# Kernel tuning notes

Measured on AMD Instinct MI355X. Metric: run time of the kernel, lower is better.

Reference implementation:

```python
import jax, jax.numpy as jnp
import numpy as np

N = 50000      # nodes
E = 600000     # edges
A = 8          # max attrs per node
DT = 64        # node type embed dim
DA = 64        # node attr embed dim
C = DT + DA    # annotation dim = GGNN channels
T = 16         # num node types
TE = 4         # num edge types
L = 4          # num_agg_steps
B = 256        # num graphs
VATTR = 1000   # num node attrs
ENC = 128      # encoder_output_dim
NCLS = 10      # decoder output classes


def setup_inputs() -> dict:
    key = jax.random.key(0)
    ks = jax.random.split(key, 16)
    s = 0.05
    x_type = jax.random.randint(ks[0], (N,), 0, T)
    x_attrs = jax.random.randint(ks[1], (N, A), 0, VATTR)
    x_attrs_mask = jax.random.randint(ks[2], (N,), 1, A + 1)  # >=1 valid attr per node
    edge_index = jax.random.randint(ks[3], (2, E), 0, N)
    edge_attr = jax.random.randint(ks[4], (E,), 0, TE)
    batch = jnp.sort(jax.random.randint(ks[5], (N,), 0, B))
    return {
        'x_type': x_type, 'x_attrs': x_attrs, 'x_attrs_mask': x_attrs_mask,
        'edge_index': edge_index, 'edge_attr': edge_attr,
        'num_graphs': int(B), 'batch': batch,
        'type_emb': jax.random.normal(ks[6], (T, DT)) * s,
        'attr_emb': jax.random.normal(ks[7], (VATTR, DA)) * s,
        'W_msg': jax.random.normal(ks[8], (L, TE, C, C)) * s,
        'W_ih': jax.random.normal(ks[9], (3 * C, C)) * s,
        'W_hh': jax.random.normal(ks[10], (3 * C, C)) * s,
        'b_ih': jnp.zeros((3 * C,)),
        'b_hh': jnp.zeros((3 * C,)),
        'w_attn': jax.random.normal(ks[11], (C,)) * s,
        'b_attn': jnp.zeros(()),
        'W_enc': jax.random.normal(ks[12], (T * C, ENC)) * s,
        'b_enc': jnp.zeros((ENC,)),
        'W_dec': jax.random.normal(ks[13], (ENC, NCLS)) * s,
        'b_dec': jnp.zeros((NCLS,)),
    }


def _gru_cell(m, h, W_ih, W_hh, b_ih, b_hh):
    gi = m @ W_ih.T + b_ih            # [N, 3C]
    gh = h @ W_hh.T + b_hh            # [N, 3C]
    ir, iz, inn = jnp.split(gi, 3, axis=-1)
    hr, hz, hn = jnp.split(gh, 3, axis=-1)
    r = jax.nn.sigmoid(ir + hr)
    z = jax.nn.sigmoid(iz + hz)
    n = jnp.tanh(inn + r * hn)
    return (1.0 - z) * n + z * h


def reference(x_type, x_attrs, x_attrs_mask, edge_index, edge_attr, num_graphs, batch,
              type_emb, attr_emb, W_msg, W_ih, W_hh, b_ih, b_hh,
              w_attn, b_attn, W_enc, b_enc, W_dec, b_dec):
    n = x_type.shape[0]
    # --- embed node types and ragged-mean attribute embeddings ---
    t_emb = type_emb[x_type]                                   # [N, DT]
    a_all = attr_emb[x_attrs]                                  # [N, A, DA]
    valid = (jnp.arange(A)[None, :] < x_attrs_mask[:, None]).astype(a_all.dtype)
    a_emb = (a_all * valid[..., None]).sum(1) / jnp.maximum(x_attrs_mask, 1)[:, None].astype(a_all.dtype)
    x = jnp.concatenate([t_emb, a_emb], axis=1)                # [N, C]

    # --- GatedGraphConv with per-edge-type weights (sum aggregation + GRU) ---
    src, dst = edge_index[0], edge_index[1]
    for l in range(L):
        h_all = jnp.einsum('nc,tcd->tnd', x, W_msg[l])         # [TE, N, C]
        m_e = h_all.reshape(TE * n, C)[edge_attr * n + src]    # [E, C] gather per edge
        m = jax.ops.segment_sum(m_e, dst, num_segments=n)      # [N, C]
        x = _gru_cell(m, x, W_ih, W_hh, b_ih, b_hh)

    # --- per-(graph, node_type) segment mean (zeros for empty groups) ---
    seg = batch * T + x_type                                   # [N]
    S = num_graphs * T
    sums = jax.ops.segment_sum(x, seg, num_segments=S)         # [B*T, C]
    cnt = jax.ops.segment_sum(jnp.ones((n,), x.dtype), seg, num_segments=S)
    agg = jnp.where(cnt[:, None] > 0, sums / jnp.maximum(cnt, 1.0)[:, None], 0.0)
    agg = agg.reshape(num_graphs, T, C)                        # [B, T, C]

    # --- attention over node types, flatten, encode, decode ---
    w = agg @ w_attn + b_attn                                  # [B, T]
    attn = jax.nn.softmax(w, axis=-1)
    flat = (attn[..., None] * agg).reshape(num_graphs, T * C)  # [B, T*C]
    enc = flat @ W_enc + b_enc                                 # [B, ENC]
    return enc @ W_dec + b_dec                                 # [B, NCLS]
```

## Files before the change

### kernel.cpp

```cpp
#include <hip/hip_runtime.h>
#include <hip/hip_bf16.h>

#define NN 50000
#define NP 50016
#define EE 600000
#define AA 8
#define CC 128
#define TT 16
#define TE 4
#define LL 4
#define BB 256
#define ENC 128
#define NCLS 10
#define SROW 136

typedef __attribute__((ext_vector_type(8))) short bf16x8;
typedef __attribute__((ext_vector_type(4))) float fx4;

__device__ __forceinline__ float b2f(ushort u) {
    union { float f; uint32_t i; } v; v.i = ((uint32_t)u) << 16; return v.f;
}
__device__ __forceinline__ ushort f2b(float f) {
    union { float f; uint32_t i; } v; v.f = f;
    uint32_t x = v.i;
    x += 0x7FFFu + ((x >> 16) & 1u);
    return (ushort)(x >> 16);
}
__device__ __forceinline__ float ldw(const void* p, long i, int isf) {
    return isf ? ((const float*)p)[i] : b2f(((const ushort*)p)[i]);
}
__device__ __forceinline__ float sigm(float t) { return 1.f / (1.f + __expf(-t)); }

__global__ void sniff_kernel(int* flag, const void* W_enc_raw) {
    const ushort* u = (const ushort*)W_enc_raw;
    int good = 0;
    for (int i = 0; i < 256; ++i) {
        ushort v = u[i];
        int ex = (v >> 7) & 0xFF;
        if (v == 0 || (ex >= 100 && ex <= 126)) ++good;
    }
    *flag = (good >= 230) ? 0 : 1;
}

__global__ __launch_bounds__(256) void wstk_kernel(ushort* __restrict__ wstk,
                                                   const void* __restrict__ W,
                                                   const int* __restrict__ flag) {
    const int isf = *flag;
    int idx = blockIdx.x * 256 + threadIdx.x;
    int l = idx >> 16;
    int rem = idx & 65535;
    int d = rem >> 9, r2 = rem & 511;
    int t = r2 >> 7, c = r2 & 127;
    long src = ((long)(l * 4 + t) << 14) + c * 128 + d;
    wstk[idx] = isf ? f2b(((const float*)W)[src]) : ((const ushort*)W)[src];
}

__global__ __launch_bounds__(256) void wgru_kernel(ushort* __restrict__ wgb,
                                                   const void* __restrict__ Wih,
                                                   const void* __restrict__ Whh,
                                                   const int* __restrict__ flag) {
    const int isf = *flag;
    int idx = blockIdx.x * 256 + threadIdx.x;
    if (idx >= 98304) return;
    int ih = (idx < 49152);
    int off = ih ? idx : idx - 49152;
    wgb[idx] = f2b(ldw(ih ? Wih : Whh, off, isf));
}

__global__ __launch_bounds__(256) void wencT_kernel(ushort* __restrict__ wencT,
                                                    const void* __restrict__ W_enc,
                                                    const int* __restrict__ flag) {
    const int isf = *flag;
    int idx = blockIdx.x * 256 + threadIdx.x;
    int j = idx >> 11, k = idx & 2047;
    wencT[idx] = f2b(ldw(W_enc, (long)k * ENC + j, isf));
}

__global__ __launch_bounds__(256) void bconv_kernel(float* __restrict__ cvt,
                                                    const void* __restrict__ bih, const void* __restrict__ bhh,
                                                    const void* __restrict__ b_enc, const void* __restrict__ w_attn,
                                                    const void* __restrict__ b_dec, const void* __restrict__ b_attn,
                                                    const void* __restrict__ W_dec,
                                                    const int* __restrict__ flag) {
    const int isf = *flag;
    int i = blockIdx.x * 256 + threadIdx.x;
    if (i < 384) cvt[i] = ldw(bih, i, isf);
    else if (i < 768) cvt[i] = ldw(bhh, i - 384, isf);
    else if (i < 896) cvt[i] = ldw(b_enc, i - 768, isf);
    else if (i < 1024) cvt[i] = ldw(w_attn, i - 896, isf);
    else if (i < 1034) cvt[i] = ldw(b_dec, i - 1024, isf);
    else if (i == 1034) cvt[i] = ldw(b_attn, 0, isf);
    else if (i >= 1040 && i < 2320) cvt[i] = ldw(W_dec, i - 1040, isf);
}

__global__ __launch_bounds__(256) void embed_kernel(
    ushort* __restrict__ xbf,
    const int* __restrict__ x_type, const int* __restrict__ x_attrs,
    const int* __restrict__ x_mask, const void* __restrict__ type_emb,
    const void* __restrict__ attr_emb, const int* __restrict__ flag) {
    const int isf = *flag;
    int idx = blockIdx.x * 256 + threadIdx.x;
    int n = idx >> 6, c = idx & 63;
    if (n >= NP) return;
    if (n >= NN) { xbf[n * CC + c] = 0; xbf[n * CC + 64 + c] = 0; return; }
    int ty = x_type[n];
    xbf[n * CC + c] = f2b(ldw(type_emb, ty * 64 + c, isf));
    int cnt = x_mask[n];
    float s = 0.f;
    for (int a = 0; a < cnt; ++a) s += ldw(attr_emb, x_attrs[n * AA + a] * 64 + c, isf);
    xbf[n * CC + 64 + c] = f2b(s / (float)cnt);
}

__global__ __launch_bounds__(256) void deg_kernel(int* __restrict__ cnt, const int* __restrict__ ei) {
    int e = blockIdx.x * 256 + threadIdx.x;
    if (e < EE) atomicAdd(&cnt[ei[EE + e]], 1);
}
__global__ __launch_bounds__(256) void scan1_kernel(int* __restrict__ cnt, int* __restrict__ btot) {
    __shared__ int s[256];
    int tid = threadIdx.x, i = blockIdx.x * 256 + tid;
    int v = (i < NN) ? cnt[i] : 0;
    s[tid] = v; __syncthreads();
    for (int off = 1; off < 256; off <<= 1) {
        int t = (tid >= off) ? s[tid - off] : 0; __syncthreads();
        s[tid] += t; __syncthreads();
    }
    if (i < NN) cnt[i] = s[tid] - v;
    if (tid == 255) btot[blockIdx.x] = s[255];
}
__global__ __launch_bounds__(256) void scan2_kernel(int* __restrict__ btot, int nb) {
    __shared__ int s[256];
    int tid = threadIdx.x;
    int v = (tid < nb) ? btot[tid] : 0;
    s[tid] = v; __syncthreads();
    for (int off = 1; off < 256; off <<= 1) {
        int t = (tid >= off) ? s[tid - off] : 0; __syncthreads();
        s[tid] += t; __syncthreads();
    }
    if (tid < nb) btot[tid] = s[tid] - v;
}
__global__ __launch_bounds__(256) void scan3_kernel(int* __restrict__ cnt, const int* __restrict__ btot) {
    int i = blockIdx.x * 256 + threadIdx.x;
    if (i < NN) cnt[i] += btot[blockIdx.x];
}
__global__ __launch_bounds__(256) void fill_kernel(uint* __restrict__ csr, int* __restrict__ cnt,
                                                   const int* __restrict__ ei, const int* __restrict__ ea) {
    int e = blockIdx.x * 256 + threadIdx.x;
    if (e >= EE) return;
    int d = ei[EE + e];
    int pos = atomicAdd(&cnt[d], 1);
    csr[pos] = (uint)ei[e] | ((uint)ea[e] << 16);
}

__global__ __launch_bounds__(256) void gather4_kernel(
    ushort* __restrict__ s4, const ushort* __restrict__ xin,
    const uint* __restrict__ csr, const int* __restrict__ endp) {
    int w = threadIdx.x >> 6, l = threadIdx.x & 63;
    int node = blockIdx.x * 4 + w;
    int start = (node == 0) ? 0 : endp[node - 1];
    int end = endp[node];
    int c0 = l * 2;
    float a0 = 0.f, b0 = 0.f, a1 = 0.f, b1 = 0.f;
    float a2 = 0.f, b2 = 0.f, a3 = 0.f, b3 = 0.f;
    for (int i = start; i < end; ++i) {
        uint pk = csr[i];
        uint src = pk & 0xFFFFu, t = pk >> 16;
        uint hv = *(const uint*)&xin[((size_t)src << 7) + c0];
        float lo = b2f((ushort)(hv & 0xFFFFu)), hf = b2f((ushort)(hv >> 16));
        if (t == 0)      { a0 += lo; b0 += hf; }
        else if (t == 1) { a1 += lo; b1 += hf; }
        else if (t == 2) { a2 += lo; b2 += hf; }
        else             { a3 += lo; b3 += hf; }
    }
    size_t base = (size_t)node << 9;
    *(uint*)&s4[base +   0 + c0] = (uint)f2b(a0) | ((uint)f2b(b0) << 16);
    *(uint*)&s4[base + 128 + c0] = (uint)f2b(a1) | ((uint)f2b(b1) << 16);
    *(uint*)&s4[base + 256 + c0] = (uint)f2b(a2) | ((uint)f2b(b2) << 16);
    *(uint*)&s4[base + 384 + c0] = (uint)f2b(a3) | ((uint)f2b(b3) << 16);
}

template <int AGG>
__global__ __launch_bounds__(256) void msggru_kernel(
    const ushort* __restrict__ xin, ushort* __restrict__ xout,
    const ushort* __restrict__ s4, const ushort* __restrict__ wstk,
    const ushort* __restrict__ wgb, const float* __restrict__ cvt,
    float* __restrict__ sums, float* __restrict__ cnta,
    const int* __restrict__ batch, const int* __restrict__ x_type) {
    __shared__ ushort m_bf[32][SROW];
    int tid = threadIdx.x;
    int w = tid >> 6, l = tid & 63;
    int node0 = blockIdx.x * 32;
    int lr = l & 15, lk = (l >> 4) * 8, hi = l >> 4;

    {
        fx4 mq[2][2];
        mq[0][0] = (fx4){0,0,0,0}; mq[0][1] = (fx4){0,0,0,0};
        mq[1][0] = (fx4){0,0,0,0}; mq[1][1] = (fx4){0,0,0,0};
        int ct0 = w * 2, ct1 = w * 2 + 1;
#pragma unroll
        for (int ks = 0; ks < 16; ++ks) {
            int ko = ks * 32 + lk;
            bf16x8 aA = *(const bf16x8*)&s4[((size_t)(node0 + lr) << 9) + ko];
            bf16x8 aB = *(const bf16x8*)&s4[((size_t)(node0 + 16 + lr) << 9) + ko];
            bf16x8 bA = *(const bf16x8*)&wstk[(size_t)(ct0 * 16 + lr) * 512 + ko];
            bf16x8 bB = *(const bf16x8*)&wstk[(size_t)(ct1 * 16 + lr) * 512 + ko];
            mq[0][0] = __builtin_amdgcn_mfma_f32_16x16x32_bf16(aA, bA, mq[0][0], 0, 0, 0);
            mq[0][1] = __builtin_amdgcn_mfma_f32_16x16x32_bf16(aB, bA, mq[0][1], 0, 0, 0);
            mq[1][0] = __builtin_amdgcn_mfma_f32_16x16x32_bf16(aA, bB, mq[1][0], 0, 0, 0);
            mq[1][1] = __builtin_amdgcn_mfma_f32_16x16x32_bf16(aB, bB, mq[1][1], 0, 0, 0);
        }
#pragma unroll
        for (int cc = 0; cc < 2; ++cc)
#pragma unroll
            for (int rt = 0; rt < 2; ++rt)
#pragma unroll
                for (int r = 0; r < 4; ++r)
                    m_bf[rt * 16 + hi * 4 + r][(w * 2 + cc) * 16 + lr] = f2b(mq[cc][rt][r]);
    }
    __syncthreads();

    bf16x8 mf[2][4], xf[2][4];
#pragma unroll
    for (int rt = 0; rt < 2; ++rt)
#pragma unroll
        for (int ks = 0; ks < 4; ++ks) {
            mf[rt][ks] = *(const bf16x8*)&m_bf[rt * 16 + lr][ks * 32 + lk];
            xf[rt][ks] = *(const bf16x8*)&xin[(size_t)(node0 + rt * 16 + lr) * CC + ks * 32 + lk];
        }
#pragma unroll
    for (int cc = 0; cc < 2; ++cc) {
        int ct = w * 2 + cc;
        int row0 = ct * 16 + lr;
        fx4 ai[3][2], ah[3][2];
#pragma unroll
        for (int s = 0; s < 3; ++s)
#pragma unroll
            for (int rt = 0; rt < 2; ++rt) { ai[s][rt] = (fx4){0,0,0,0}; ah[s][rt] = (fx4){0,0,0,0}; }
#pragma unroll
        for (int ks = 0; ks < 4; ++ks) {
            int ko = ks * 32 + lk;
            bf16x8 bI[3], bH[3];
#pragma unroll
            for (int s = 0; s < 3; ++s) {
                bI[s] = *(const bf16x8*)&wgb[(size_t)(s * 128 + row0) * 128 + ko];
                bH[s] = *(const bf16x8*)&wgb[49152 + (size_t)(s * 128 + row0) * 128 + ko];
            }
#pragma unroll
            for (int s = 0; s < 3; ++s)
#pragma unroll
                for (int rt = 0; rt < 2; ++rt) {
                    ai[s][rt] = __builtin_amdgcn_mfma_f32_16x16x32_bf16(mf[rt][ks], bI[s], ai[s][rt], 0, 0, 0);
                    ah[s][rt] = __builtin_amdgcn_mfma_f32_16x16x32_bf16(xf[rt][ks], bH[s], ah[s][rt], 0, 0, 0);
                }
        }
        float bi0 = cvt[row0],        bh0 = cvt[384 + row0];
        float bi1 = cvt[128 + row0],  bh1 = cvt[512 + row0];
        float bi2 = cvt[256 + row0],  bh2 = cvt[640 + row0];
#pragma unroll
        for (int rt = 0; rt < 2; ++rt)
#pragma unroll
            for (int r = 0; r < 4; ++r) {
                int node = node0 + rt * 16 + hi * 4 + r;
                if (node >= NN) continue;
                float rg = sigm(ai[0][rt][r] + bi0 + ah[0][rt][r] + bh0);
                float zg = sigm(ai[1][rt][r] + bi1 + ah[1][rt][r] + bh1);
                float ny = ai[2][rt][r] + bi2 + rg * (ah[2][rt][r] + bh2);
                float ng = 2.f * sigm(2.f * ny) - 1.f;
                size_t xi = (size_t)node * CC + row0;
                float xo = b2f(xin[xi]);
                float xn = (1.f - zg) * ng + zg * xo;
                xout[xi] = f2b(xn);
                if (AGG) {
                    int seg = batch[node] * TT + x_type[node];
                    atomicAdd(&sums[(size_t)seg * CC + row0], xn);
                    if (row0 == 0) atomicAdd(&cnta[seg], 1.0f);
                }
            }
    }
}

__global__ __launch_bounds__(256) void attnflat_kernel(
    ushort* __restrict__ flatbf, const float* __restrict__ sums, const float* __restrict__ cnt,
    const float* __restrict__ cvt) {
    __shared__ float agg_s[TT][CC + 1];
    __shared__ float wpart[TT][8];
    __shared__ float attn_s[TT];
    int b = blockIdx.x, tid = threadIdx.x;
#pragma unroll
    for (int q = 0; q < 8; ++q) {
        int idx = tid + q * 256;
        int t = idx >> 7, c = idx & 127;
        float cv = cnt[b * TT + t];
        agg_s[t][c] = cv > 0.f ? sums[(size_t)(b * TT + t) * CC + c] / cv : 0.f;
    }
    __syncthreads();
    if (tid < 128) {
        int t = tid >> 3, p = tid & 7;
        float acc = 0.f;
        for (int i = 0; i < 16; ++i) acc += agg_s[t][p * 16 + i] * cvt[896 + p * 16 + i];
        wpart[t][p] = acc;
    }
    __syncthreads();
    if (tid < 16) {
        float acc = cvt[1034];
        for (int p = 0; p < 8; ++p) acc += wpart[tid][p];
        attn_s[tid] = acc;
    }
    __syncthreads();
    if (tid == 0) {
        float mx = attn_s[0];
        for (int t = 1; t < TT; ++t) mx = fmaxf(mx, attn_s[t]);
        float ssum = 0.f, ex[TT];
        for (int t = 0; t < TT; ++t) { ex[t] = __expf(attn_s[t] - mx); ssum += ex[t]; }
        for (int t = 0; t < TT; ++t) attn_s[t] = ex[t] / ssum;
    }
    __syncthreads();
#pragma unroll
    for (int q = 0; q < 8; ++q) {
        int idx = tid + q * 256;
        int t = idx >> 7, c = idx & 127;
        flatbf[(size_t)b * 2048 + idx] = f2b(agg_s[t][c] * attn_s[t]);
    }
}

__global__ __launch_bounds__(256) void enc_mfma(
    float* __restrict__ encp, const ushort* __restrict__ flatbf, const ushort* __restrict__ wencT) {
    int tid = threadIdx.x;
    int w = tid >> 6, l = tid & 63;
    int bid = blockIdx.x;
    int m0 = (bid >> 2) * 16;
    int kc = (bid & 3) * 512;
    int lr = l & 15, lk = (l >> 4) * 8;
    fx4 acc0 = {0,0,0,0}, acc1 = {0,0,0,0};
    int ct0 = w * 2, ct1 = w * 2 + 1;
#pragma unroll
    for (int ks = 0; ks < 16; ++ks) {
        int ko = kc + ks * 32 + lk;
        bf16x8 af = *(const bf16x8*)&flatbf[(size_t)(m0 + lr) * 2048 + ko];
        bf16x8 b0 = *(const bf16x8*)&wencT[(size_t)(ct0 * 16 + lr) * 2048 + ko];
        bf16x8 b1 = *(const bf16x8*)&wencT[(size_t)(ct1 * 16 + lr) * 2048 + ko];
        acc0 = __builtin_amdgcn_mfma_f32_16x16x32_bf16(af, b0, acc0, 0, 0, 0);
        acc1 = __builtin_amdgcn_mfma_f32_16x16x32_bf16(af, b1, acc1, 0, 0, 0);
    }
#pragma unroll
    for (int r = 0; r < 4; ++r) {
        int row = m0 + (l >> 4) * 4 + r;
        encp[(size_t)(bid & 3) * BB * ENC + (size_t)row * ENC + ct0 * 16 + lr] = acc0[r];
        encp[(size_t)(bid & 3) * BB * ENC + (size_t)row * ENC + ct1 * 16 + lr] = acc1[r];
    }
}

__global__ __launch_bounds__(256) void dec_kernel(
    void* __restrict__ out, const float* __restrict__ encp, const float* __restrict__ cvt,
    const int* __restrict__ flag) {
    const int isf = *flag;
    __shared__ float encs[ENC];
    int b = blockIdx.x, tid = threadIdx.x;
    if (tid < 128) {
        float e = cvt[768 + tid];
#pragma unroll
        for (int p = 0; p < 4; ++p) e += encp[(size_t)p * BB * ENC + (size_t)b * ENC + tid];
        encs[tid] = e;
    }
    __syncthreads();
    if (tid < NCLS) {
        float acc = cvt[1024 + tid];
        for (int j = 0; j < ENC; ++j) acc += encs[j] * cvt[1040 + j * NCLS + tid];
        int oi = b * NCLS + tid;
        if (isf) ((float*)out)[oi] = acc;
        else ((ushort*)out)[oi] = f2b(acc);
    }
}

extern "C" void kernel_launch(void* const* d_in, const int* in_sizes, int n_in,
                              void* d_out, int out_size, void* d_ws, size_t ws_size,
                              hipStream_t stream) {
    const int* x_type      = (const int*)d_in[0];
    const int* x_attrs     = (const int*)d_in[1];
    const int* x_mask      = (const int*)d_in[2];
    const int* edge_index  = (const int*)d_in[3];
    const int* edge_attr   = (const int*)d_in[4];
    const int* batch       = (const int*)d_in[6];
    const void* type_emb   = d_in[7];
    const void* attr_emb   = d_in[8];
    const void* W_msg      = d_in[9];
    const void* W_ih       = d_in[10];
    const void* W_hh       = d_in[11];
    const void* b_ih       = d_in[12];
    const void* b_hh       = d_in[13];
    const void* w_attn     = d_in[14];
    const void* b_attn     = d_in[15];
    const void* W_enc      = d_in[16];
    const void* b_enc      = d_in[17];
    const void* W_dec      = d_in[18];
    const void* b_dec      = d_in[19];

    char* p = (char*)d_ws;
    ushort* xbf0  = (ushort*)p;          p += (size_t)NP * CC * 2;
    ushort* xbf1  = (ushort*)p;          p += (size_t)NP * CC * 2;
    ushort* s4    = (ushort*)p;          p += (size_t)NP * 512 * 2;
    ushort* wstk  = (ushort*)p;          p += (size_t)LL * 128 * 512 * 2;
    ushort* wgb   = (ushort*)p;          p += (size_t)2 * 384 * 128 * 2;
    ushort* wencT = (ushort*)p;          p += (size_t)ENC * 2048 * 2;
    ushort* flatbf= (ushort*)p;          p += (size_t)BB * 2048 * 2;
    float*  encp  = (float*)p;           p += (size_t)4 * BB * ENC * 4;
    float*  cvt   = (float*)p;           p += 2320 * 4;
    float*  sums  = (float*)p;           p += (size_t)BB * TT * CC * 4;
    float*  cnta  = (float*)p;           p += (size_t)BB * TT * 4;
    uint*   csr   = (uint*)p;            p += (size_t)EE * 4;
    int*    cptr  = (int*)p;             p += (size_t)NN * 4;
    int*    btot  = (int*)p;             p += 256 * 4;
    int*    flag  = (int*)p;

    sniff_kernel<<<1, 1, 0, stream>>>(flag, W_enc);
    wstk_kernel<<<1024, 256, 0, stream>>>(wstk, W_msg, flag);
    wgru_kernel<<<384, 256, 0, stream>>>(wgb, W_ih, W_hh, flag);
    wencT_kernel<<<1024, 256, 0, stream>>>(wencT, W_enc, flag);
    bconv_kernel<<<10, 256, 0, stream>>>(cvt, b_ih, b_hh, b_enc, w_attn, b_dec, b_attn, W_dec, flag);
    embed_kernel<<<(NP * 64) / 256, 256, 0, stream>>>(xbf0, x_type, x_attrs, x_mask,
                                                      type_emb, attr_emb, flag);

    const int NB = (NN + 255) / 256;
    hipMemsetAsync(cptr, 0, (size_t)NN * sizeof(int), stream);
    deg_kernel<<<(EE + 255) / 256, 256, 0, stream>>>(cptr, edge_index);
    scan1_kernel<<<NB, 256, 0, stream>>>(cptr, btot);
    scan2_kernel<<<1, 256, 0, stream>>>(btot, NB);
    scan3_kernel<<<NB, 256, 0, stream>>>(cptr, btot);
    fill_kernel<<<(EE + 255) / 256, 256, 0, stream>>>(csr, cptr, edge_index, edge_attr);

    hipMemsetAsync(sums, 0, (size_t)(BB * TT * CC + BB * TT) * sizeof(float), stream);

    const int tile_grid = NP / 32;
    for (int l = 0; l < LL; ++l) {
        const ushort* xin = (l & 1) ? xbf1 : xbf0;
        ushort* xout      = (l & 1) ? xbf0 : xbf1;
        gather4_kernel<<<NN / 4, 256, 0, stream>>>(s4, xin, csr, cptr);
        const ushort* wl = wstk + (size_t)l * 128 * 512;
        if (l < LL - 1)
            msggru_kernel<0><<<tile_grid, 256, 0, stream>>>(xin, xout, s4, wl, wgb, cvt,
                                                            sums, cnta, batch, x_type);
        else
            msggru_kernel<1><<<tile_grid, 256, 0, stream>>>(xin, xout, s4, wl, wgb, cvt,
                                                            sums, cnta, batch, x_type);
    }

    attnflat_kernel<<<BB, 256, 0, stream>>>(flatbf, sums, cnta, cvt);
    enc_mfma<<<64, 256, 0, stream>>>(encp, flatbf, wencT);
    dec_kernel<<<BB, 256, 0, stream>>>(d_out, encp, cvt, flag);
}
```

Baseline: 840.8 us.

## Stage s4 tile in LDS, XCD-swizzle block order, unroll edge gather by two

The message-GRU kernel now copies the 32x512 s4 tile for its block into shared memory once, so the MFMA A operands are read from LDS instead of being fetched repeatedly from global memory by all four waves. Both the gather and the msggru kernels remap block IDs with an XCD-aware swizzle so that adjacent node blocks land on the same XCD, which should improve L2 locality. The gather loop processes two edges per iteration to expose more independent loads. In exchange, the kernel uses about 33KB of extra LDS, which may reduce occupancy, and adds a barrier before the compute.

```diff
diff --git a/kernel.cpp b/kernel.cpp
--- a/kernel.cpp
+++ b/kernel.cpp
@@ -13,6 +13,7 @@
 #define ENC 128
 #define NCLS 10
 #define SROW 136
+#define STR 520
 
 typedef __attribute__((ext_vector_type(8))) short bf16x8;
 typedef __attribute__((ext_vector_type(4))) float fx4;
@@ -30,6 +31,11 @@
     return isf ? ((const float*)p)[i] : b2f(((const ushort*)p)[i]);
 }
 __device__ __forceinline__ float sigm(float t) { return 1.f / (1.f + __expf(-t)); }
+
+__device__ __forceinline__ int xcd_swz(int bid, int nwg) {
+    int q = nwg >> 3, r = nwg & 7, x = bid & 7, o = bid >> 3;
+    return (x < r ? x * (q + 1) : r * (q + 1) + (x - r) * q) + o;
+}
 
 __global__ void sniff_kernel(int* flag, const void* W_enc_raw) {
     const ushort* u = (const ushort*)W_enc_raw;
@@ -155,13 +161,32 @@
     ushort* __restrict__ s4, const ushort* __restrict__ xin,
     const uint* __restrict__ csr, const int* __restrict__ endp) {
     int w = threadIdx.x >> 6, l = threadIdx.x & 63;
-    int node = blockIdx.x * 4 + w;
+    int wg = xcd_swz(blockIdx.x, NN / 4);
+    int node = wg * 4 + w;
     int start = (node == 0) ? 0 : endp[node - 1];
     int end = endp[node];
     int c0 = l * 2;
     float a0 = 0.f, b0 = 0.f, a1 = 0.f, b1 = 0.f;
     float a2 = 0.f, b2 = 0.f, a3 = 0.f, b3 = 0.f;
-    for (int i = start; i < end; ++i) {
+    int i = start;
+    for (; i + 1 < end; i += 2) {
+        uint pkA = csr[i], pkB = csr[i + 1];
+        uint srcA = pkA & 0xFFFFu, tA = pkA >> 16;
+        uint srcB = pkB & 0xFFFFu, tB = pkB >> 16;
+        uint hvA = *(const uint*)&xin[((size_t)srcA << 7) + c0];
+        uint hvB = *(const uint*)&xin[((size_t)srcB << 7) + c0];
+        float loA = b2f((ushort)(hvA & 0xFFFFu)), hfA = b2f((ushort)(hvA >> 16));
+        float loB = b2f((ushort)(hvB & 0xFFFFu)), hfB = b2f((ushort)(hvB >> 16));
+        if (tA == 0)      { a0 += loA; b0 += hfA; }
+        else if (tA == 1) { a1 += loA; b1 += hfA; }
+        else if (tA == 2) { a2 += loA; b2 += hfA; }
+        else              { a3 += loA; b3 += hfA; }
+        if (tB == 0)      { a0 += loB; b0 += hfB; }
+        else if (tB == 1) { a1 += loB; b1 += hfB; }
+        else if (tB == 2) { a2 += loB; b2 += hfB; }
+        else              { a3 += loB; b3 += hfB; }
+    }
+    if (i < end) {
         uint pk = csr[i];
         uint src = pk & 0xFFFFu, t = pk >> 16;
         uint hv = *(const uint*)&xin[((size_t)src << 7) + c0];
@@ -185,10 +210,25 @@
     const ushort* __restrict__ wgb, const float* __restrict__ cvt,
     float* __restrict__ sums, float* __restrict__ cnta,
     const int* __restrict__ batch, const int* __restrict__ x_type) {
+    __shared__ ushort s_tile[32][STR];
     __shared__ ushort m_bf[32][SROW];
     int tid = threadIdx.x;
+    int wg = xcd_swz(blockIdx.x, NP / 32);
+    int node0 = wg * 32;
+
+    {
+        const ushort* src = &s4[(size_t)node0 << 9];
+#pragma unroll
+        for (int q = 0; q < 8; ++q) {
+            int i8 = (q * 256 + tid) * 8;
+            int n = i8 >> 9, c = i8 & 511;
+            bf16x8 v = *(const bf16x8*)&src[i8];
+            *(bf16x8*)&s_tile[n][c] = v;
+        }
+    }
+    __syncthreads();
+
     int w = tid >> 6, l = tid & 63;
-    int node0 = blockIdx.x * 32;
     int lr = l & 15, lk = (l >> 4) * 8, hi = l >> 4;
 
     {
@@ -199,8 +239,8 @@
 #pragma unroll
         for (int ks = 0; ks < 16; ++ks) {
             int ko = ks * 32 + lk;
-            bf16x8 aA = *(const bf16x8*)&s4[((size_t)(node0 + lr) << 9) + ko];
-            bf16x8 aB = *(const bf16x8*)&s4[((size_t)(node0 + 16 + lr) << 9) + ko];
+            bf16x8 aA = *(const bf16x8*)&s_tile[lr][ko];
+            bf16x8 aB = *(const bf16x8*)&s_tile[16 + lr][ko];
             bf16x8 bA = *(const bf16x8*)&wstk[(size_t)(ct0 * 16 + lr) * 512 + ko];
             bf16x8 bB = *(const bf16x8*)&wstk[(size_t)(ct1 * 16 + lr) * 512 + ko];
             mq[0][0] = __builtin_amdgcn_mfma_f32_16x16x32_bf16(aA, bA, mq[0][0], 0, 0, 0);
```

Result: faster. 689.6 us (-18.0%).
